# Kernel optimization log

Hardware: AMD Instinct MI355X
Metric: run time of the kernel (lower is better)

Reference implementation:

```python
import jax, jax.numpy as jnp
import numpy as np

N, E = 50000, 600000
DIN, D, C = 239, 128, 2
NEG_SLOPE_MLP = 0.01   # nn.LeakyReLU default
NEG_SLOPE_ATT = 0.2    # GATConv default


def leaky(x, s):
    return jnp.where(x >= 0, x, s * x)


def setup_inputs() -> dict:
    key = jax.random.key(0)
    ks = jax.random.split(key, 12)
    sc = lambda d: 1.0 / np.sqrt(d)
    return {
        "x": jax.random.normal(ks[0], (N, DIN), jnp.float32),
        "edge_index": jax.random.randint(ks[1], (2, E), 0, N, jnp.int32),
        "edge_type": jax.random.randint(ks[2], (E,), 0, 4, jnp.int32),
        "W_in": jax.random.normal(ks[3], (DIN, D), jnp.float32) * sc(DIN),
        "b_in": jnp.zeros((D,), jnp.float32),
        "W_gat": jax.random.normal(ks[4], (D, D), jnp.float32) * sc(D),
        "att_src": jax.random.normal(ks[5], (D,), jnp.float32) * sc(D),
        "att_dst": jax.random.normal(ks[6], (D,), jnp.float32) * sc(D),
        "b_gat": jnp.zeros((D,), jnp.float32),
        "W_h": jax.random.normal(ks[7], (D, D), jnp.float32) * sc(D),
        "b_h": jnp.zeros((D,), jnp.float32),
        "W_out": jax.random.normal(ks[8], (D, C), jnp.float32) * sc(D),
        "b_out": jnp.zeros((C,), jnp.float32),
    }


def reference(x, edge_index, edge_type, W_in, b_in, W_gat, att_src, att_dst,
              b_gat, W_h, b_h, W_out, b_out):
    # input encoder: Linear + LeakyReLU
    h = leaky(x @ W_in + b_in, NEG_SLOPE_MLP)                      # [N, D]

    # GATConv (heads=1): add self loops, edge attention, segment softmax over dst
    loops = jnp.arange(N, dtype=edge_index.dtype)
    src = jnp.concatenate([edge_index[0], loops])                  # [E+N]
    dst = jnp.concatenate([edge_index[1], loops])

    g = h @ W_gat                                                  # [N, D]
    a_src = g @ att_src                                            # [N]
    a_dst = g @ att_dst                                            # [N]
    e = leaky(a_src[src] + a_dst[dst], NEG_SLOPE_ATT)              # [E+N]

    m = jax.ops.segment_max(e, dst, num_segments=N)                # self-loops => no empty segs
    w = jnp.exp(e - m[dst])
    z = jax.ops.segment_sum(w, dst, num_segments=N)
    alpha = w / z[dst]                                             # [E+N]

    out = jax.ops.segment_sum(alpha[:, None] * g[src], dst, num_segments=N) + b_gat

    # dropout is identity in eval mode
    h2 = leaky(out @ W_h + b_h, NEG_SLOPE_MLP)
    return h2 @ W_out + b_out                                      # [N, C]
```

## Files before the change

### kernel.cpp

```cpp
#include <hip/hip_runtime.h>

#define NNODE 50000
#define NEDGE 600000
#define KDIN  239
#define DDIM  128
#define NTILES 3125
#define NBG   782
#define NBUCK 256
#define BSZ   196
#define NPB   128
#define CHP   4688

typedef _Float16 half8 __attribute__((ext_vector_type(8)));
typedef _Float16 half4 __attribute__((ext_vector_type(4)));
typedef __attribute__((ext_vector_type(4))) float f32x4;

__device__ __forceinline__ ushort f2h(float f){
  union { _Float16 h; ushort u; } c; c.h = (_Float16)f; return c.u;
}

__global__ __launch_bounds__(256) void pre_k(
    const float* __restrict__ W_in, const float* __restrict__ W_gat, const float* __restrict__ W_h,
    ushort* __restrict__ BfA, ushort* __restrict__ BfB, ushort* __restrict__ BfC,
    const int* __restrict__ ei, int* __restrict__ cpart)
{
  __shared__ int hb[NBUCK];
  const int b = blockIdx.x, t = threadIdx.x;
  if (b < NPB){
    hb[t] = 0;
    __syncthreads();
    const int e0 = b*CHP, e1 = min(NEDGE, e0+CHP);
    for (int e=e0+t; e<e1; e+=256){
      int dst = min(max(ei[NEDGE+e],0), NNODE-1);
      atomicAdd(&hb[dst/BSZ], 1);
    }
    __syncthreads();
    cpart[b*NBUCK + t] = hb[t];
  } else if (b < NPB + 128){
    int idx = (b-NPB)*256 + t; int n = idx >> 8, k = idx & 255;
    BfA[idx] = (k < KDIN) ? f2h(W_in[(size_t)k*DDIM + n]) : (ushort)0;
  } else if (b < NPB + 192){
    int idx = (b-NPB-128)*256 + t; int n = idx >> 7, k = idx & 127;
    BfB[idx] = f2h(W_gat[(size_t)k*DDIM + n]);
  } else {
    int idx = (b-NPB-192)*256 + t; int n = idx >> 7, k = idx & 127;
    BfC[idx] = f2h(W_h[(size_t)k*DDIM + n]);
  }
}

__global__ __launch_bounds__(256) void scan_k(int* __restrict__ cpart)
{
  __shared__ int sc[NBUCK];
  const int t = threadIdx.x;
  int tot = 0;
  #pragma unroll 8
  for (int i=0;i<NPB;i++) tot += cpart[i*NBUCK + t];
  sc[t] = tot;
  __syncthreads();
  #pragma unroll
  for (int off=1; off<NBUCK; off<<=1){
    int v = (t>=off) ? sc[t-off] : 0;
    __syncthreads();
    sc[t] += v;
    __syncthreads();
  }
  int run = sc[t] - tot;
  #pragma unroll 8
  for (int i=0;i<NPB;i++){
    int c = cpart[i*NBUCK + t];
    cpart[i*NBUCK + t] = run;
    run += c;
  }
}

__global__ __launch_bounds__(256, 2) void gemmAB_k(
    const float* __restrict__ x, const ushort* __restrict__ BfA,
    const ushort* __restrict__ BfB, const float* __restrict__ b_in,
    ushort* __restrict__ gf,
    const float* __restrict__ vs, const float* __restrict__ vd,
    float* __restrict__ os, float* __restrict__ od,
    float* __restrict__ bms, float* __restrict__ bmd,
    const int* __restrict__ ei, const int* __restrict__ cpart, int* __restrict__ pairs)
{
  __shared__ __attribute__((aligned(16))) ushort Bs[128*256];
  __shared__ __attribute__((aligned(16))) ushort ht[4][16*128];
  if (blockIdx.x < NPB){
    int* cur = (int*)Bs;
    const int pb = blockIdx.x;
    cur[threadIdx.x] = cpart[pb*NBUCK + threadIdx.x];
    __syncthreads();
    const int e0 = pb*CHP, e1 = min(NEDGE, e0+CHP);
    for (int e=e0+threadIdx.x; e<e1; e+=256){
      int dst = min(max(ei[NEDGE+e],0), NNODE-1);
      int src = min(max(ei[e],0), NNODE-1);
      int bk = (unsigned)dst / BSZ;
      int pos = atomicAdd(&cur[bk], 1);
      pairs[pos] = src | ((dst - bk*BSZ) << 16);
    }
    return;
  }
  #pragma unroll
  for (int it=0; it<16; ++it){
    const int idx = it*256 + threadIdx.x;
    const int row = idx >> 5, sl = (idx & 31)*16;
    const half8 v = *(const half8*)(BfA + (size_t)idx*8);
    *(half8*)((char*)Bs + row*512 + (sl ^ ((row&7)<<4))) = v;
  }
  __syncthreads();
  const int lane = threadIdx.x & 63;
  const int wave = threadIdx.x >> 6;
  const int q = lane >> 4, c = lane & 15;
  const int tile = (blockIdx.x - NPB)*4 + wave;
  const bool act = tile < NTILES;
  const int rowBase = tile*16;
  const int swz = (c&7)<<4;
  f32x4 acc[8];
  if (act){
    const float* __restrict__ ap = x + (size_t)(rowBase + c)*KDIN;
    half8 af[8];
    #pragma unroll
    for (int s=0;s<7;s++){
      const float* __restrict__ p = ap + s*32 + q*8;
      #pragma unroll
      for (int i=0;i<8;i++) af[s][i] = (_Float16)p[i];
    }
    #pragma unroll
    for (int i=0;i<8;i++){
      const int k = 224 + q*8 + i;
      af[7][i] = (_Float16)((k < KDIN) ? ap[k] : 0.f);
    }
    #pragma unroll
    for (int t=0;t<8;t++) acc[t] = (f32x4){0.f,0.f,0.f,0.f};
    const char* __restrict__ bsl = (const char*)Bs + c*512;
    #pragma unroll
    for (int s=0;s<8;s++){
      const int so = (s*64 + q*16) ^ swz;
      #pragma unroll
      for (int t=0;t<8;t++){
        const half8 bf = *(const half8*)(bsl + t*16*512 + so);
        acc[t] = __builtin_amdgcn_mfma_f32_16x16x32_f16(af[s], bf, acc[t], 0,0,0);
      }
    }
    char* __restrict__ hw = (char*)&ht[wave][0];
    #pragma unroll
    for (int t=0;t<8;t++){
      const int col = 16*t + c;
      const float bv = b_in[col];
      #pragma unroll
      for (int r=0;r<4;r++){
        const int row = q*4 + r;
        float v = acc[t][r] + bv;
        v = (v >= 0.f) ? v : 0.01f*v;
        *(_Float16*)(hw + ((row*256 + col*2) ^ ((row&7)<<4))) = (_Float16)v;
      }
    }
  }
  __syncthreads();
  #pragma unroll
  for (int it=0; it<8; ++it){
    const int idx = it*256 + threadIdx.x;
    const int row = idx >> 4, sl = (idx & 15)*16;
    const half8 v = *(const half8*)(BfB + (size_t)idx*8);
    *(half8*)((char*)Bs + row*256 + (sl ^ ((row&7)<<4))) = v;
  }
  __syncthreads();
  if (!act) return;
  half8 af2[4];
  const char* __restrict__ hr = (const char*)&ht[wave][0] + c*256;
  #pragma unroll
  for (int s=0;s<4;s++) af2[s] = *(const half8*)(hr + ((s*64 + q*16) ^ swz));
  #pragma unroll
  for (int t=0;t<8;t++) acc[t] = (f32x4){0.f,0.f,0.f,0.f};
  const char* __restrict__ bsl2 = (const char*)Bs + c*256;
  #pragma unroll
  for (int s=0;s<4;s++){
    const int so = (s*64 + q*16) ^ swz;
    #pragma unroll
    for (int t=0;t<8;t++){
      const half8 bf = *(const half8*)(bsl2 + t*16*256 + so);
      acc[t] = __builtin_amdgcn_mfma_f32_16x16x32_f16(af2[s], bf, acc[t], 0,0,0);
    }
  }
  float pr0[4] = {0,0,0,0}, pr1[4] = {0,0,0,0};
  #pragma unroll
  for (int t=0;t<8;t++){
    const int col = 16*t + c;
    const float va = vs[col], vb = vd[col];
    #pragma unroll
    for (int r=0;r<4;r++){
      const int row = rowBase + q*4 + r;
      const float v = acc[t][r];
      gf[(size_t)row*DDIM + col] = f2h(v);
      pr0[r] += v*va; pr1[r] += v*vb;
    }
  }
  float lmax_s = -3.0e38f, lmax_d = -3.0e38f;
  #pragma unroll
  for (int r=0;r<4;r++){
    float s0 = pr0[r], s1 = pr1[r];
    s0 += __shfl_xor(s0,8); s1 += __shfl_xor(s1,8);
    s0 += __shfl_xor(s0,4); s1 += __shfl_xor(s1,4);
    s0 += __shfl_xor(s0,2); s1 += __shfl_xor(s1,2);
    s0 += __shfl_xor(s0,1); s1 += __shfl_xor(s1,1);
    lmax_s = fmaxf(lmax_s, s0); lmax_d = fmaxf(lmax_d, s1);
    if (c == 0){
      const int row = rowBase + q*4 + r;
      os[row] = s0; od[row] = s1;
    }
  }
  #pragma unroll
  for (int off=32; off>0; off>>=1){
    lmax_s = fmaxf(lmax_s, __shfl_xor(lmax_s, off));
    lmax_d = fmaxf(lmax_d, __shfl_xor(lmax_d, off));
  }
  if (lane == 0){ bms[tile] = lmax_s; bmd[tile] = lmax_d; }
}

__global__ __launch_bounds__(256, 4) void gemmC_k(
    const ushort* __restrict__ Af, const ushort* __restrict__ Btf,
    const float* __restrict__ bias, float* __restrict__ outf,
    const float* __restrict__ Wo, const float* __restrict__ bo)
{
  constexpr int Kpad = 128, Kb = 256;
  __shared__ __attribute__((aligned(16))) ushort Bs[128*Kpad];
  #pragma unroll
  for (int it=0; it<8; ++it){
    const int idx = it*256 + threadIdx.x;
    const int row = idx >> 4, sl = (idx & 15)*16;
    const half8 v = *(const half8*)(Btf + (size_t)idx*8);
    *(half8*)((char*)Bs + row*Kb + (sl ^ ((row&7)<<4))) = v;
  }
  __syncthreads();
  const int lane = threadIdx.x & 63;
  const int wave = threadIdx.x >> 6;
  const int q = lane >> 4, c = lane & 15;
  const int tile = blockIdx.x*4 + wave;
  if (tile >= NTILES) return;
  const int rowBase = tile*16;
  half8 af[4];
  const ushort* __restrict__ ap = Af + (size_t)(rowBase + c)*Kpad + q*8;
  #pragma unroll
  for (int s=0;s<4;s++) af[s] = *(const half8*)(ap + s*32);
  f32x4 acc[8];
  #pragma unroll
  for (int t=0;t<8;t++) acc[t] = (f32x4){0.f,0.f,0.f,0.f};
  const int swz = (c&7)<<4;
  const char* __restrict__ bsl = (const char*)Bs + c*Kb;
  #pragma unroll
  for (int s=0;s<4;s++){
    const int so = (s*64 + q*16) ^ swz;
    #pragma unroll
    for (int t=0;t<8;t++){
      const half8 bf = *(const half8*)(bsl + t*16*Kb + so);
      acc[t] = __builtin_amdgcn_mfma_f32_16x16x32_f16(af[s], bf, acc[t], 0,0,0);
    }
  }
  float pr0[4] = {0,0,0,0}, pr1[4] = {0,0,0,0};
  #pragma unroll
  for (int t=0;t<8;t++){
    const int col = 16*t + c;
    const float bv = bias[col];
    const float va = Wo[2*col], vb = Wo[2*col+1];
    #pragma unroll
    for (int r=0;r<4;r++){
      float v = acc[t][r] + bv;
      v = (v >= 0.f) ? v : 0.01f*v;
      pr0[r] += v*va; pr1[r] += v*vb;
    }
  }
  #pragma unroll
  for (int r=0;r<4;r++){
    float s0 = pr0[r], s1 = pr1[r];
    s0 += __shfl_xor(s0,8); s1 += __shfl_xor(s1,8);
    s0 += __shfl_xor(s0,4); s1 += __shfl_xor(s1,4);
    s0 += __shfl_xor(s0,2); s1 += __shfl_xor(s1,2);
    s0 += __shfl_xor(s0,1); s1 += __shfl_xor(s1,1);
    if (c == 0){
      const int row = rowBase + q*4 + r;
      float2 y2; y2.x = s0 + bo[0]; y2.y = s1 + bo[1];
      *(float2*)&outf[(size_t)row*2] = y2;
    }
  }
}

__global__ __launch_bounds__(256) void fine_k(const int* __restrict__ pairs,
    const int* __restrict__ cpart, int* __restrict__ offs, int* __restrict__ degv,
    int* __restrict__ es, const float* __restrict__ bms, const float* __restrict__ bmd,
    float* __restrict__ gmf)
{
  __shared__ int fh[256];
  __shared__ int sc[256];
  const int b = blockIdx.x, t = threadIdx.x;
  if (b == NBUCK){
    float ms = -3.0e38f, md = -3.0e38f;
    for (int i=t; i<NTILES; i+=256){ ms = fmaxf(ms, bms[i]); md = fmaxf(md, bmd[i]); }
    #pragma unroll
    for (int off=32; off>0; off>>=1){
      ms = fmaxf(ms, __shfl_xor(ms, off));
      md = fmaxf(md, __shfl_xor(md, off));
    }
    float* red = (float*)fh;
    const int w = t >> 6;
    if ((t & 63) == 0){ red[w] = ms; red[4+w] = md; }
    __syncthreads();
    if (t == 0){
      gmf[0] = fmaxf(fmaxf(red[0],red[1]), fmaxf(red[2],red[3]));
      gmf[1] = fmaxf(fmaxf(red[4],red[5]), fmaxf(red[6],red[7]));
    }
    return;
  }
  const int s0 = cpart[b];
  const int s1 = (b < NBUCK-1) ? cpart[b+1] : NEDGE;
  fh[t] = 0;
  __syncthreads();
  for (int i=s0+t; i<s1; i+=256)
    atomicAdd(&fh[pairs[i] >> 16], 1);
  __syncthreads();
  const int deg = fh[t];
  sc[t] = deg;
  __syncthreads();
  #pragma unroll
  for (int off=1; off<256; off<<=1){
    int v = (t>=off) ? sc[t-off] : 0;
    __syncthreads();
    sc[t] += v;
    __syncthreads();
  }
  const int excl = sc[t] - deg;
  const int dst = b*BSZ + t;
  if (t < BSZ && dst < NNODE){ offs[dst] = s0 + excl; degv[dst] = deg; }
  fh[t] = s0 + excl;
  __syncthreads();
  for (int i=s0+t; i<s1; i+=256){
    const int p = pairs[i];
    const int pos = atomicAdd(&fh[p >> 16], 1);
    es[pos] = p & 0xFFFF;
  }
}

__global__ __launch_bounds__(256) void agg_k(const ushort* __restrict__ gf,
    const int* __restrict__ offs, const int* __restrict__ degv,
    const int* __restrict__ es,
    const float* __restrict__ a_src, const float* __restrict__ a_dst,
    const float* __restrict__ gmf, const float* __restrict__ b_gat,
    ushort* __restrict__ og)
{
  const int lane = threadIdx.x & 63;
  const int half = lane >> 5, li = lane & 31;
  const int dst = blockIdx.x*8 + (threadIdx.x >> 6)*2 + half;
  if (dst >= NNODE) return;
  float M = gmf[0] + gmf[1];
  M = (M >= 0.f) ? M : 0.2f*M;
  const int start = offs[dst];
  const int deg = degv[dst];
  const int* __restrict__ bin = es + start;
  const float ad = a_dst[dst];
  f32x4 a0={0,0,0,0}, a1={0,0,0,0}, a2={0,0,0,0}, a3={0,0,0,0};
  float w0s=0.f, w1s=0.f, w2s=0.f, w3s=0.f;
  int j = 0;
  for (; j+3 < deg; j += 4){
    const int i0=bin[j], i1=bin[j+1], i2=bin[j+2], i3=bin[j+3];
    float e0=a_src[i0]+ad; e0=(e0>=0.f)?e0:0.2f*e0;
    float e1=a_src[i1]+ad; e1=(e1>=0.f)?e1:0.2f*e1;
    float e2=a_src[i2]+ad; e2=(e2>=0.f)?e2:0.2f*e2;
    float e3=a_src[i3]+ad; e3=(e3>=0.f)?e3:0.2f*e3;
    const float w0=__expf(e0-M), w1=__expf(e1-M), w2=__expf(e2-M), w3=__expf(e3-M);
    const half4 g0 = *(const half4*)(gf + (size_t)i0*DDIM + li*4);
    const half4 g1 = *(const half4*)(gf + (size_t)i1*DDIM + li*4);
    const half4 g2 = *(const half4*)(gf + (size_t)i2*DDIM + li*4);
    const half4 g3 = *(const half4*)(gf + (size_t)i3*DDIM + li*4);
    #pragma unroll
    for (int i=0;i<4;i++){
      a0[i] += w0*(float)g0[i]; a1[i] += w1*(float)g1[i];
      a2[i] += w2*(float)g2[i]; a3[i] += w3*(float)g3[i];
    }
    w0s += w0; w1s += w1; w2s += w2; w3s += w3;
  }
  for (; j < deg; ++j){
    const int si = bin[j];
    float e0=a_src[si]+ad; e0=(e0>=0.f)?e0:0.2f*e0;
    const float w = __expf(e0-M);
    const half4 gv = *(const half4*)(gf + (size_t)si*DDIM + li*4);
    #pragma unroll
    for (int i=0;i<4;i++) a0[i] += w*(float)gv[i];
    w0s += w;
  }
  {
    float evs=a_src[dst]+ad; evs=(evs>=0.f)?evs:0.2f*evs;
    const float w = __expf(evs-M);
    const half4 gv = *(const half4*)(gf + (size_t)dst*DDIM + li*4);
    #pragma unroll
    for (int i=0;i<4;i++) a0[i] += w*(float)gv[i];
    w0s += w;
  }
  const float inv = 1.f/(w0s+w1s+w2s+w3s);
  const float4 bg = *(const float4*)&b_gat[li*4];
  ushort4 o;
  o.x = f2h((a0[0]+a1[0]+a2[0]+a3[0])*inv + bg.x);
  o.y = f2h((a0[1]+a1[1]+a2[1]+a3[1])*inv + bg.y);
  o.z = f2h((a0[2]+a1[2]+a2[2]+a3[2])*inv + bg.z);
  o.w = f2h((a0[3]+a1[3]+a2[3]+a3[3])*inv + bg.w);
  *(ushort4*)(og + (size_t)dst*DDIM + li*4) = o;
}

extern "C" void kernel_launch(void* const* d_in, const int* in_sizes, int n_in,
                              void* d_out, int out_size, void* d_ws, size_t ws_size,
                              hipStream_t stream)
{
  const float* x       = (const float*)d_in[0];
  const int*   ei      = (const int*)d_in[1];
  const float* W_in    = (const float*)d_in[3];
  const float* b_in    = (const float*)d_in[4];
  const float* W_gat   = (const float*)d_in[5];
  const float* att_src = (const float*)d_in[6];
  const float* att_dst = (const float*)d_in[7];
  const float* b_gat   = (const float*)d_in[8];
  const float* W_h     = (const float*)d_in[9];
  const float* b_h     = (const float*)d_in[10];
  const float* W_out   = (const float*)d_in[11];
  const float* b_out   = (const float*)d_in[12];

  char* ws = (char*)d_ws;
  ushort*   gf     = (ushort*)  (ws + 12800000);
  ushort*   og     = (ushort*)  (ws + 25600000);
  ushort*   BfA    = (ushort*)  (ws + 38400000);
  ushort*   BfB    = (ushort*)  (ws + 38600000);
  ushort*   BfC    = (ushort*)  (ws + 38700000);
  int*      cpart  = (int*)     (ws + 38800000);
  int*      pairs  = (int*)     (ws + 39100000);
  int*      es     = (int*)     (ws + 41500000);
  int*      offs   = (int*)     (ws + 43900000);
  int*      degv   = (int*)     (ws + 44100000);
  float*    a_src  = (float*)   (ws + 44300000);
  float*    a_dst  = (float*)   (ws + 44500000);
  float*    gm     = (float*)   (ws + 44700000);
  float*    bmaxS  = (float*)   (ws + 44700032);
  float*    bmaxD  = (float*)   (ws + 44712544);

  pre_k<<<NPB + 256, 256, 0, stream>>>(W_in, W_gat, W_h, BfA, BfB, BfC, ei, cpart);
  scan_k<<<1, 256, 0, stream>>>(cpart);
  gemmAB_k<<<NPB + NBG, 256, 0, stream>>>(x, BfA, BfB, b_in, gf,
      att_src, att_dst, a_src, a_dst, bmaxS, bmaxD, ei, cpart, pairs);
  fine_k<<<NBUCK + 1, 256, 0, stream>>>(pairs, cpart, offs, degv, es, bmaxS, bmaxD, gm);
  agg_k<<<6250, 256, 0, stream>>>(gf, offs, degv, es, a_src, a_dst, gm, b_gat, og);
  gemmC_k<<<NBG, 256, 0, stream>>>(og, BfC, b_h, (float*)d_out, W_out, b_out);
}
```

Before: 183.3 us.

## Fuse bucket sort and aggregation, fold scan and max via last-block tickets

Removes the separate scan kernel by having the last histogram block in pre_k (chosen through an atomic ticket counter) do the bucket prefix scan. The global max reduction moves into the last GEMM block of gemmAB_k the same way. fine_k and agg_k are merged into one 1024-thread-per-bucket kernel that builds each bucket's CSR in shared memory and aggregates from it, so the es/offs/degv arrays no longer round-trip through global memory. In exchange it adds a memset for the tickets and serial tail work in the last block. Aggregation also drops to 256 blocks with fewer waves in flight for the latency-bound gather.

Measured after the change: 267.0 us. +45.7%, slower.

```diff
diff --git a/kernel.cpp b/kernel.cpp
--- a/kernel.cpp
+++ b/kernel.cpp
@@ -10,6 +10,7 @@
 #define BSZ   196
 #define NPB   128
 #define CHP   4688
+#define ESCAP 4096
 
 typedef _Float16 half8 __attribute__((ext_vector_type(8)));
 typedef _Float16 half4 __attribute__((ext_vector_type(4)));
@@ -22,9 +23,10 @@
 __global__ __launch_bounds__(256) void pre_k(
     const float* __restrict__ W_in, const float* __restrict__ W_gat, const float* __restrict__ W_h,
     ushort* __restrict__ BfA, ushort* __restrict__ BfB, ushort* __restrict__ BfC,
-    const int* __restrict__ ei, int* __restrict__ cpart)
+    const int* __restrict__ ei, int* __restrict__ cpart, unsigned* __restrict__ ticks)
 {
   __shared__ int hb[NBUCK];
+  __shared__ unsigned lastv;
   const int b = blockIdx.x, t = threadIdx.x;
   if (b < NPB){
     hb[t] = 0;
@@ -36,6 +38,30 @@
     }
     __syncthreads();
     cpart[b*NBUCK + t] = hb[t];
+    __threadfence();
+    if (t == 0) lastv = atomicAdd(&ticks[0], 1u);
+    __syncthreads();
+    if (lastv == NPB-1){
+      __threadfence();
+      volatile int* cp = cpart;
+      int tot = 0;
+      for (int i=0;i<NPB;i++) tot += cp[i*NBUCK + t];
+      hb[t] = tot;
+      __syncthreads();
+      #pragma unroll
+      for (int off=1; off<NBUCK; off<<=1){
+        int v = (t>=off) ? hb[t-off] : 0;
+        __syncthreads();
+        hb[t] += v;
+        __syncthreads();
+      }
+      int run = hb[t] - tot;
+      for (int i=0;i<NPB;i++){
+        int c = cp[i*NBUCK + t];
+        cpart[i*NBUCK + t] = run;
+        run += c;
+      }
+    }
   } else if (b < NPB + 128){
     int idx = (b-NPB)*256 + t; int n = idx >> 8, k = idx & 255;
     BfA[idx] = (k < KDIN) ? f2h(W_in[(size_t)k*DDIM + n]) : (ushort)0;
@@ -48,31 +74,6 @@
   }
 }
 
-__global__ __launch_bounds__(256) void scan_k(int* __restrict__ cpart)
-{
-  __shared__ int sc[NBUCK];
-  const int t = threadIdx.x;
-  int tot = 0;
-  #pragma unroll 8
-  for (int i=0;i<NPB;i++) tot += cpart[i*NBUCK + t];
-  sc[t] = tot;
-  __syncthreads();
-  #pragma unroll
-  for (int off=1; off<NBUCK; off<<=1){
-    int v = (t>=off) ? sc[t-off] : 0;
-    __syncthreads();
-    sc[t] += v;
-    __syncthreads();
-  }
-  int run = sc[t] - tot;
-  #pragma unroll 8
-  for (int i=0;i<NPB;i++){
-    int c = cpart[i*NBUCK + t];
-    cpart[i*NBUCK + t] = run;
-    run += c;
-  }
-}
-
 __global__ __launch_bounds__(256, 2) void gemmAB_k(
     const float* __restrict__ x, const ushort* __restrict__ BfA,
     const ushort* __restrict__ BfB, const float* __restrict__ b_in,
@@ -80,10 +81,12 @@
     const float* __restrict__ vs, const float* __restrict__ vd,
     float* __restrict__ os, float* __restrict__ od,
     float* __restrict__ bms, float* __restrict__ bmd,
-    const int* __restrict__ ei, const int* __restrict__ cpart, int* __restrict__ pairs)
+    const int* __restrict__ ei, const int* __restrict__ cpart, int* __restrict__ pairs,
+    float* __restrict__ gmf, unsigned* __restrict__ ticks)
 {
   __shared__ __attribute__((aligned(16))) ushort Bs[128*256];
   __shared__ __attribute__((aligned(16))) ushort ht[4][16*128];
+  __shared__ unsigned lastg;
   if (blockIdx.x < NPB){
     int* cur = (int*)Bs;
     const int pb = blockIdx.x;
@@ -164,56 +167,184 @@
     *(half8*)((char*)Bs + row*256 + (sl ^ ((row&7)<<4))) = v;
   }
   __syncthreads();
-  if (!act) return;
-  half8 af2[4];
-  const char* __restrict__ hr = (const char*)&ht[wave][0] + c*256;
-  #pragma unroll
-  for (int s=0;s<4;s++) af2[s] = *(const half8*)(hr + ((s*64 + q*16) ^ swz));
-  #pragma unroll
-  for (int t=0;t<8;t++) acc[t] = (f32x4){0.f,0.f,0.f,0.f};
-  const char* __restrict__ bsl2 = (const char*)Bs + c*256;
-  #pragma unroll
-  for (int s=0;s<4;s++){
-    const int so = (s*64 + q*16) ^ swz;
+  if (act){
+    half8 af2[4];
+    const char* __restrict__ hr = (const char*)&ht[wave][0] + c*256;
+    #pragma unroll
+    for (int s=0;s<4;s++) af2[s] = *(const half8*)(hr + ((s*64 + q*16) ^ swz));
+    #pragma unroll
+    for (int t=0;t<8;t++) acc[t] = (f32x4){0.f,0.f,0.f,0.f};
+    const char* __restrict__ bsl2 = (const char*)Bs + c*256;
+    #pragma unroll
+    for (int s=0;s<4;s++){
+      const int so = (s*64 + q*16) ^ swz;
+      #pragma unroll
+      for (int t=0;t<8;t++){
+        const half8 bf = *(const half8*)(bsl2 + t*16*256 + so);
+        acc[t] = __builtin_amdgcn_mfma_f32_16x16x32_f16(af2[s], bf, acc[t], 0,0,0);
+      }
+    }
+    float pr0[4] = {0,0,0,0}, pr1[4] = {0,0,0,0};
     #pragma unroll
     for (int t=0;t<8;t++){
-      const half8 bf = *(const half8*)(bsl2 + t*16*256 + so);
-      acc[t] = __builtin_amdgcn_mfma_f32_16x16x32_f16(af2[s], bf, acc[t], 0,0,0);
-    }
-  }
-  float pr0[4] = {0,0,0,0}, pr1[4] = {0,0,0,0};
-  #pragma unroll
-  for (int t=0;t<8;t++){
-    const int col = 16*t + c;
-    const float va = vs[col], vb = vd[col];
+      const int col = 16*t + c;
+      const float va = vs[col], vb = vd[col];
+      #pragma unroll
+      for (int r=0;r<4;r++){
+        const int row = rowBase + q*4 + r;
+        const float v = acc[t][r];
+        gf[(size_t)row*DDIM + col] = f2h(v);
+        pr0[r] += v*va; pr1[r] += v*vb;
+      }
+    }
+    float lmax_s = -3.0e38f, lmax_d = -3.0e38f;
     #pragma unroll
     for (int r=0;r<4;r++){
-      const int row = rowBase + q*4 + r;
-      const float v = acc[t][r];
-      gf[(size_t)row*DDIM + col] = f2h(v);
-      pr0[r] += v*va; pr1[r] += v*vb;
-    }
-  }
-  float lmax_s = -3.0e38f, lmax_d = -3.0e38f;
-  #pragma unroll
-  for (int r=0;r<4;r++){
-    float s0 = pr0[r], s1 = pr1[r];
-    s0 += __shfl_xor(s0,8); s1 += __shfl_xor(s1,8);
-    s0 += __shfl_xor(s0,4); s1 += __shfl_xor(s1,4);
-    s0 += __shfl_xor(s0,2); s1 += __shfl_xor(s1,2);
-    s0 += __shfl_xor(s0,1); s1 += __shfl_xor(s1,1);
-    lmax_s = fmaxf(lmax_s, s0); lmax_d = fmaxf(lmax_d, s1);
-    if (c == 0){
-      const int row = rowBase + q*4 + r;
-      os[row] = s0; od[row] = s1;
-    }
-  }
-  #pragma unroll
-  for (int off=32; off>0; off>>=1){
-    lmax_s = fmaxf(lmax_s, __shfl_xor(lmax_s, off));
-    lmax_d = fmaxf(lmax_d, __shfl_xor(lmax_d, off));
-  }
-  if (lane == 0){ bms[tile] = lmax_s; bmd[tile] = lmax_d; }
+      float s0 = pr0[r], s1 = pr1[r];
+      s0 += __shfl_xor(s0,8); s1 += __shfl_xor(s1,8);
+      s0 += __shfl_xor(s0,4); s1 += __shfl_xor(s1,4);
+      s0 += __shfl_xor(s0,2); s1 += __shfl_xor(s1,2);
+      s0 += __shfl_xor(s0,1); s1 += __shfl_xor(s1,1);
+      lmax_s = fmaxf(lmax_s, s0); lmax_d = fmaxf(lmax_d, s1);
+      if (c == 0){
+        const int row = rowBase + q*4 + r;
+        os[row] = s0; od[row] = s1;
+      }
+    }
+    #pragma unroll
+    for (int off=32; off>0; off>>=1){
+      lmax_s = fmaxf(lmax_s, __shfl_xor(lmax_s, off));
+      lmax_d = fmaxf(lmax_d, __shfl_xor(lmax_d, off));
+    }
+    if (lane == 0){ bms[tile] = lmax_s; bmd[tile] = lmax_d; }
+  }
+  __syncthreads();
+  if (threadIdx.x == 0){ __threadfence(); lastg = atomicAdd(&ticks[1], 1u); }
+  __syncthreads();
+  if (lastg == NBG-1){
+    __threadfence();
+    volatile float* pS = bms; volatile float* pD = bmd;
+    float ms = -3.0e38f, md = -3.0e38f;
+    for (int i=threadIdx.x; i<NTILES; i+=256){ ms = fmaxf(ms, pS[i]); md = fmaxf(md, pD[i]); }
+    #pragma unroll
+    for (int off=32; off>0; off>>=1){
+      ms = fmaxf(ms, __shfl_xor(ms, off));
+      md = fmaxf(md, __shfl_xor(md, off));
+    }
+    float* red = (float*)ht;
+    if (lane == 0){ red[wave] = ms; red[4+wave] = md; }
+    __syncthreads();
+    if (threadIdx.x == 0){
+      gmf[0] = fmaxf(fmaxf(red[0],red[1]), fmaxf(red[2],red[3]));
+      gmf[1] = fmaxf(fmaxf(red[4],red[5]), fmaxf(red[6],red[7]));
+    }
+  }
+}
+
+__global__ __launch_bounds__(1024, 1) void fineagg_k(
+    const int* __restrict__ pairs, const int* __restrict__ cpart,
+    int* __restrict__ es, const ushort* __restrict__ gf,
+    const float* __restrict__ a_src, const float* __restrict__ a_dst,
+    const float* __restrict__ gmf, const float* __restrict__ b_gat,
+    ushort* __restrict__ og)
+{
+  __shared__ int fh[256];
+  __shared__ int sc2[256];
+  __shared__ int offL[256];
+  __shared__ int degL[256];
+  __shared__ int esL[ESCAP];
+  const int b = blockIdx.x, t = threadIdx.x;
+  const int s0 = cpart[b];
+  const int s1 = (b < NBUCK-1) ? cpart[b+1] : NEDGE;
+  const bool fit = (s1 - s0) <= ESCAP;
+  if (t < 256) fh[t] = 0;
+  __syncthreads();
+  for (int i=s0+t; i<s1; i+=1024)
+    atomicAdd(&fh[pairs[i] >> 16], 1);
+  __syncthreads();
+  int deg = 0;
+  if (t < 256){ deg = fh[t]; sc2[t] = deg; }
+  __syncthreads();
+  #pragma unroll
+  for (int off=1; off<256; off<<=1){
+    int v = (t < 256 && t >= off) ? sc2[t-off] : 0;
+    __syncthreads();
+    if (t < 256) sc2[t] += v;
+    __syncthreads();
+  }
+  if (t < 256){
+    const int excl = sc2[t] - deg;
+    offL[t] = s0 + excl;
+    degL[t] = deg;
+    fh[t] = s0 + excl;
+  }
+  __syncthreads();
+  for (int i=s0+t; i<s1; i+=1024){
+    const int p = pairs[i];
+    const int pos = atomicAdd(&fh[p >> 16], 1);
+    if (fit) esL[pos - s0] = p & 0xFFFF;
+    else     es[pos] = p & 0xFFFF;
+  }
+  __syncthreads();
+  float M = gmf[0] + gmf[1];
+  M = (M >= 0.f) ? M : 0.2f*M;
+  const int lane = t & 63;
+  const int half = lane >> 5, li = lane & 31;
+  const int slot = (t >> 6)*2 + half;
+  for (int d = slot; d < BSZ; d += 32){
+    const int dst = b*BSZ + d;
+    if (dst >= NNODE) continue;
+    const int start = offL[d];
+    const int dg = degL[d];
+    const int* __restrict__ bin = fit ? (const int*)(esL + (start - s0)) : (es + start);
+    const float ad = a_dst[dst];
+    f32x4 a0={0,0,0,0}, a1={0,0,0,0}, a2={0,0,0,0}, a3={0,0,0,0};
+    float w0s=0.f, w1s=0.f, w2s=0.f, w3s=0.f;
+    int j = 0;
+    for (; j+3 < dg; j += 4){
+      const int i0=bin[j], i1=bin[j+1], i2=bin[j+2], i3=bin[j+3];
+      float e0=a_src[i0]+ad; e0=(e0>=0.f)?e0:0.2f*e0;
+      float e1=a_src[i1]+ad; e1=(e1>=0.f)?e1:0.2f*e1;
+      float e2=a_src[i2]+ad; e2=(e2>=0.f)?e2:0.2f*e2;
+      float e3=a_src[i3]+ad; e3=(e3>=0.f)?e3:0.2f*e3;
+      const float w0=__expf(e0-M), w1=__expf(e1-M), w2=__expf(e2-M), w3=__expf(e3-M);
+      const half4 g0 = *(const half4*)(gf + (size_t)i0*DDIM + li*4);
+      const half4 g1 = *(const half4*)(gf + (size_t)i1*DDIM + li*4);
+      const half4 g2 = *(const half4*)(gf + (size_t)i2*DDIM + li*4);
+      const half4 g3 = *(const half4*)(gf + (size_t)i3*DDIM + li*4);
+      #pragma unroll
+      for (int i=0;i<4;i++){
+        a0[i] += w0*(float)g0[i]; a1[i] += w1*(float)g1[i];
+        a2[i] += w2*(float)g2[i]; a3[i] += w3*(float)g3[i];
+      }
+      w0s += w0; w1s += w1; w2s += w2; w3s += w3;
+    }
+    for (; j < dg; ++j){
+      const int si = bin[j];
+      float e0=a_src[si]+ad; e0=(e0>=0.f)?e0:0.2f*e0;
+      const float w = __expf(e0-M);
+      const half4 gv = *(const half4*)(gf + (size_t)si*DDIM + li*4);
+      #pragma unroll
+      for (int i=0;i<4;i++) a0[i] += w*(float)gv[i];
+      w0s += w;
+    }
+    {
+      float evs=a_src[dst]+ad; evs=(evs>=0.f)?evs:0.2f*evs;
+      const float w = __expf(evs-M);
+      const half4 gv = *(const half4*)(gf + (size_t)dst*DDIM + li*4);
+      #pragma unroll
+      for (int i=0;i<4;i++) a0[i] += w*(float)gv[i];
+      w0s += w;
+    }
+    const float inv = 1.f/(w0s+w1s+w2s+w3s);
+    const float4 bg = *(const float4*)&b_gat[li*4];
+    ushort4 o;
+    o.x = f2h((a0[0]+a1[0]+a2[0]+a3[0])*inv + bg.x);
+    o.y = f2h((a0[1]+a1[1]+a2[1]+a3[1])*inv + bg.y);
+    o.z = f2h((a0[2]+a1[2]+a2[2]+a3[2])*inv + bg.z);
+    o.w = f2h((a0[3]+a1[3]+a2[3]+a3[3])*inv + bg.w);
+    *(ushort4*)(og + (size_t)dst*DDIM + li*4) = o;
+  }
 }
 
 __global__ __launch_bounds__(256, 4) void gemmC_k(
@@ -281,126 +412,6 @@
       *(float2*)&outf[(size_t)row*2] = y2;
     }
   }
-}
-
-__global__ __launch_bounds__(256) void fine_k(const int* __restrict__ pairs,
-    const int* __restrict__ cpart, int* __restrict__ offs, int* __restrict__ degv,
-    int* __restrict__ es, const float* __restrict__ bms, const float* __restrict__ bmd,
-    float* __restrict__ gmf)
-{
-  __shared__ int fh[256];
-  __shared__ int sc[256];
-  const int b = blockIdx.x, t = threadIdx.x;
-  if (b == NBUCK){
-    float ms = -3.0e38f, md = -3.0e38f;
-    for (int i=t; i<NTILES; i+=256){ ms = fmaxf(ms, bms[i]); md = fmaxf(md, bmd[i]); }
-    #pragma unroll
-    for (int off=32; off>0; off>>=1){
-      ms = fmaxf(ms, __shfl_xor(ms, off));
-      md = fmaxf(md, __shfl_xor(md, off));
-    }
-    float* red = (float*)fh;
-    const int w = t >> 6;
-    if ((t & 63) == 0){ red[w] = ms; red[4+w] = md; }
-    __syncthreads();
-    if (t == 0){
-      gmf[0] = fmaxf(fmaxf(red[0],red[1]), fmaxf(red[2],red[3]));
-      gmf[1] = fmaxf(fmaxf(red[4],red[5]), fmaxf(red[6],red[7]));
-    }
-    return;
-  }
-  const int s0 = cpart[b];
-  const int s1 = (b < NBUCK-1) ? cpart[b+1] : NEDGE;
-  fh[t] = 0;
-  __syncthreads();
-  for (int i=s0+t; i<s1; i+=256)
-    atomicAdd(&fh[pairs[i] >> 16], 1);
-  __syncthreads();
-  const int deg = fh[t];
-  sc[t] = deg;
-  __syncthreads();
-  #pragma unroll
-  for (int off=1; off<256; off<<=1){
-    int v = (t>=off) ? sc[t-off] : 0;
-    __syncthreads();
-    sc[t] += v;
-    __syncthreads();
-  }
-  const int excl = sc[t] - deg;
-  const int dst = b*BSZ + t;
-  if (t < BSZ && dst < NNODE){ offs[dst] = s0 + excl; degv[dst] = deg; }
-  fh[t] = s0 + excl;
-  __syncthreads();
-  for (int i=s0+t; i<s1; i+=256){
-    const int p = pairs[i];
-    const int pos = atomicAdd(&fh[p >> 16], 1);
-    es[pos] = p & 0xFFFF;
-  }
-}
-
-__global__ __launch_bounds__(256) void agg_k(const ushort* __restrict__ gf,
-    const int* __restrict__ offs, const int* __restrict__ degv,
-    const int* __restrict__ es,
-    const float* __restrict__ a_src, const float* __restrict__ a_dst,
-    const float* __restrict__ gmf, const float* __restrict__ b_gat,
-    ushort* __restrict__ og)
-{
-  const int lane = threadIdx.x & 63;
-  const int half = lane >> 5, li = lane & 31;
-  const int dst = blockIdx.x*8 + (threadIdx.x >> 6)*2 + half;
-  if (dst >= NNODE) return;
-  float M = gmf[0] + gmf[1];
-  M = (M >= 0.f) ? M : 0.2f*M;
-  const int start = offs[dst];
-  const int deg = degv[dst];
-  const int* __restrict__ bin = es + start;
-  const float ad = a_dst[dst];
-  f32x4 a0={0,0,0,0}, a1={0,0,0,0}, a2={0,0,0,0}, a3={0,0,0,0};
-  float w0s=0.f, w1s=0.f, w2s=0.f, w3s=0.f;
-  int j = 0;
-  for (; j+3 < deg; j += 4){
-    const int i0=bin[j], i1=bin[j+1], i2=bin[j+2], i3=bin[j+3];
-    float e0=a_src[i0]+ad; e0=(e0>=0.f)?e0:0.2f*e0;
-    float e1=a_src[i1]+ad; e1=(e1>=0.f)?e1:0.2f*e1;
-    float e2=a_src[i2]+ad; e2=(e2>=0.f)?e2:0.2f*e2;
-    float e3=a_src[i3]+ad; e3=(e3>=0.f)?e3:0.2f*e3;
-    const float w0=__expf(e0-M), w1=__expf(e1-M), w2=__expf(e2-M), w3=__expf(e3-M);
-    const half4 g0 = *(const half4*)(gf + (size_t)i0*DDIM + li*4);
-    const half4 g1 = *(const half4*)(gf + (size_t)i1*DDIM + li*4);
-    const half4 g2 = *(const half4*)(gf + (size_t)i2*DDIM + li*4);
-    const half4 g3 = *(const half4*)(gf + (size_t)i3*DDIM + li*4);
-    #pragma unroll
-    for (int i=0;i<4;i++){
-      a0[i] += w0*(float)g0[i]; a1[i] += w1*(float)g1[i];
-      a2[i] += w2*(float)g2[i]; a3[i] += w3*(float)g3[i];
-    }
-    w0s += w0; w1s += w1; w2s += w2; w3s += w3;
-  }
-  for (; j < deg; ++j){
-    const int si = bin[j];
-    float e0=a_src[si]+ad; e0=(e0>=0.f)?e0:0.2f*e0;
-    const float w = __expf(e0-M);
-    const half4 gv = *(const half4*)(gf + (size_t)si*DDIM + li*4);
-    #pragma unroll
-    for (int i=0;i<4;i++) a0[i] += w*(float)gv[i];
-    w0s += w;
-  }
-  {
-    float evs=a_src[dst]+ad; evs=(evs>=0.f)?evs:0.2f*evs;
-    const float w = __expf(evs-M);
-    const half4 gv = *(const half4*)(gf + (size_t)dst*DDIM + li*4);
-    #pragma unroll
-    for (int i=0;i<4;i++) a0[i] += w*(float)gv[i];
-    w0s += w;
-  }
-  const float inv = 1.f/(w0s+w1s+w2s+w3s);
-  const float4 bg = *(const float4*)&b_gat[li*4];
-  ushort4 o;
-  o.x = f2h((a0[0]+a1[0]+a2[0]+a3[0])*inv + bg.x);
-  o.y = f2h((a0[1]+a1[1]+a2[1]+a3[1])*inv + bg.y);
-  o.z = f2h((a0[2]+a1[2]+a2[2]+a3[2])*inv + bg.z);
-  o.w = f2h((a0[3]+a1[3]+a2[3]+a3[3])*inv + bg.w);
-  *(ushort4*)(og + (size_t)dst*DDIM + li*4) = o;
 }
 
 extern "C" void kernel_launch(void* const* d_in, const int* in_sizes, int n_in,
@@ -421,27 +432,25 @@
   const float* b_out   = (const float*)d_in[12];
 
   char* ws = (char*)d_ws;
-  ushort*   gf     = (ushort*)  (ws + 12800000);
-  ushort*   og     = (ushort*)  (ws + 25600000);
-  ushort*   BfA    = (ushort*)  (ws + 38400000);
-  ushort*   BfB    = (ushort*)  (ws + 38600000);
-  ushort*   BfC    = (ushort*)  (ws + 38700000);
-  int*      cpart  = (int*)     (ws + 38800000);
-  int*      pairs  = (int*)     (ws + 39100000);
-  int*      es     = (int*)     (ws + 41500000);
-  int*      offs   = (int*)     (ws + 43900000);
-  int*      degv   = (int*)     (ws + 44100000);
-  float*    a_src  = (float*)   (ws + 44300000);
-  float*    a_dst  = (float*)   (ws + 44500000);
-  float*    gm     = (float*)   (ws + 44700000);
-  float*    bmaxS  = (float*)   (ws + 44700032);
-  float*    bmaxD  = (float*)   (ws + 44712544);
-
-  pre_k<<<NPB + 256, 256, 0, stream>>>(W_in, W_gat, W_h, BfA, BfB, BfC, ei, cpart);
-  scan_k<<<1, 256, 0, stream>>>(cpart);
+  ushort*   gf     = (ushort*)  (ws + 0);
+  ushort*   og     = (ushort*)  (ws + 12800000);
+  ushort*   BfA    = (ushort*)  (ws + 25600000);
+  ushort*   BfB    = (ushort*)  (ws + 25800000);
+  ushort*   BfC    = (ushort*)  (ws + 25900000);
+  int*      cpart  = (int*)     (ws + 26000000);
+  int*      pairs  = (int*)     (ws + 26300000);
+  int*      es     = (int*)     (ws + 28700000);
+  float*    a_src  = (float*)   (ws + 31100000);
+  float*    a_dst  = (float*)   (ws + 31300000);
+  float*    gm     = (float*)   (ws + 31500000);
+  unsigned* ticks  = (unsigned*)(ws + 31500064);
+  float*    bmaxS  = (float*)   (ws + 31600000);
+  float*    bmaxD  = (float*)   (ws + 31616000);
+
+  hipMemsetAsync(ticks, 0, 8, stream);
+  pre_k<<<NPB + 256, 256, 0, stream>>>(W_in, W_gat, W_h, BfA, BfB, BfC, ei, cpart, ticks);
   gemmAB_k<<<NPB + NBG, 256, 0, stream>>>(x, BfA, BfB, b_in, gf,
-      att_src, att_dst, a_src, a_dst, bmaxS, bmaxD, ei, cpart, pairs);
-  fine_k<<<NBUCK + 1, 256, 0, stream>>>(pairs, cpart, offs, degv, es, bmaxS, bmaxD, gm);
-  agg_k<<<6250, 256, 0, stream>>>(gf, offs, degv, es, a_src, a_dst, gm, b_gat, og);
+      att_src, att_dst, a_src, a_dst, bmaxS, bmaxD, ei, cpart, pairs, gm, ticks);
+  fineagg_k<<<NBUCK, 1024, 0, stream>>>(pairs, cpart, es, gf, a_src, a_dst, gm, b_gat, og);
   gemmC_k<<<NBG, 256, 0, stream>>>(og, BfC, b_h, (float*)d_out, W_out, b_out);
 }
```
